# Optimization experiments

Measured on AMD Instinct MI355X. Metric: run time of the kernel, lower is better.

The kernel has to match this reference:

```python
import jax, jax.numpy as jnp
import numpy as np

N_NODES = 100000
N_EDGES = 1600000
DIM = 64

def setup_inputs() -> dict:
    key = jax.random.key(0)
    k1, k2, k3 = jax.random.split(key, 3)
    x = jax.random.normal(k1, (N_NODES, DIM), dtype=jnp.float32)
    edge_index = jax.random.randint(k2, (2, N_EDGES), 0, N_NODES, dtype=jnp.int64)
    edge_weight = jax.random.uniform(k3, (N_EDGES,), dtype=jnp.float32)
    return {"x": x, "edge_index": edge_index, "edge_weight": edge_weight}

def reference(x, edge_index, edge_weight):
    # out[row] += x[col] * edge_weight  (edge-weighted gather + scatter-add)
    row, col = edge_index[0], edge_index[1]
    messages = x[col] * edge_weight[:, None]            # [E, dim]
    out = jax.ops.segment_sum(messages, row, num_segments=x.shape[0])  # [N, dim]
    return out
```

## Files before the change

### kernel.cpp

```cpp
#include <hip/hip_runtime.h>
#include <hip/hip_fp16.h>
#include <stdint.h>


typedef unsigned long long ull;
typedef int   v4i __attribute__((ext_vector_type(4)));
typedef float v4f __attribute__((ext_vector_type(4)));

#define RB      64
#define CAP     1280
#define CHUNK   2048
#define SLOTS   48
#define BPAD    16
#define OVF_CAP 65536
#define MAXNB   2048

__device__ __forceinline__ unsigned short f2bf(float f) {
    union { float f; unsigned int u; } c;
    c.f = f;
    unsigned int lsb = (c.u >> 16) & 1u;
    c.u += 0x7fffu + lsb;
    return (unsigned short)(c.u >> 16);
}
__device__ __forceinline__ float bf2f(unsigned short u) {
    union { unsigned int u; float f; } c;
    c.u = ((unsigned int)u) << 16;
    return c.f;
}
__device__ __forceinline__ unsigned pack_cw(int col, float w) {
    unsigned hb = __half_as_ushort(__float2half(w));
    return (((unsigned)col) << 15) | (hb >> 1);
}
__device__ __forceinline__ float unpack_w(unsigned v) {
    return __half2float(__ushort_as_half((unsigned short)((v & 0x7fffu) << 1)));
}

__global__ __launch_bounds__(512) void prep(
    const int* __restrict__ ei, const float* __restrict__ ew,
    int* __restrict__ bcnt, ull* __restrict__ seg,
    int* __restrict__ ovf_cnt, int3* __restrict__ ovf, int E, int NB,
    int nbin, const float* __restrict__ x, unsigned short* __restrict__ xb,
    int n4)
{
    __shared__ int hist[MAXNB];
    __shared__ int gbase[MAXNB];
    int t = threadIdx.x;

    if ((int)blockIdx.x >= nbin) {
        int i0 = ((int)blockIdx.x - nbin) * 2048 + t;
#pragma unroll
        for (int k = 0; k < 4; ++k) {
            int i = i0 + k * 512;
            if (i < n4) {
                v4f v = ((const v4f*)x)[i];
                ushort4 o;
                o.x = f2bf(v.x); o.y = f2bf(v.y);
                o.z = f2bf(v.z); o.w = f2bf(v.w);
                ((ushort4*)xb)[i] = o;
            }
        }
        return;
    }

    for (int i = t; i < NB; i += 512) hist[i] = 0;
    __syncthreads();

    int e0 = blockIdx.x * CHUNK;
    int eb = e0 + t * 4;
    bool al4 = ((E & 3) == 0);

    unsigned pk[4];
    ull      cw[4];
    bool     vd[4];
    {
        v4i r4, c4; v4f w4;
        if (al4 && eb + 3 < E) {
            r4 = *(const v4i*)(ei + eb);
            c4 = *(const v4i*)(ei + E + eb);
            w4 = *(const v4f*)(ew + eb);
        } else {
#pragma unroll
            for (int u = 0; u < 4; ++u) {
                int e = eb + u;
                r4[u] = e < E ? ei[e] : 0;
                c4[u] = e < E ? ei[E + e] : 0;
                w4[u] = e < E ? ew[e] : 0.f;
            }
        }
#pragma unroll
        for (int u = 0; u < 4; ++u) {
            int e = eb + u;
            vd[u] = e < E;
            int bkt = r4[u] >> 6;
            int rl  = r4[u] & (RB - 1);
            int lp = 0;
            if (vd[u]) lp = atomicAdd(&hist[bkt], 1);
            pk[u] = (((unsigned)lp) << 11) | (unsigned)bkt;
            cw[u] = (((ull)__float_as_uint(w4[u])) << 32) |
                    (unsigned)((rl << 17) | c4[u]);
        }
    }
    __syncthreads();

    for (int i = t; i < NB; i += 512) {
        int h = hist[i];
        gbase[i] = h ? atomicAdd(&bcnt[i * BPAD], h) : 0;
    }
    __syncthreads();

#pragma unroll
    for (int j = 0; j < 4; ++j) {
        if (!vd[j]) continue;
        int bkt = pk[j] & 2047;
        int pos = gbase[bkt] + (int)(pk[j] >> 11);
        if (pos < CAP) {
            seg[(size_t)bkt * CAP + pos] = cw[j];
        } else {
            int o = atomicAdd(ovf_cnt, 1);
            if (o < OVF_CAP) {
                unsigned lo = (unsigned)cw[j];
                ovf[o] = make_int3((bkt << 6) | ((lo >> 17) & (RB - 1)),
                                   lo & 0x1FFFF, (int)(cw[j] >> 32));
            }
        }
    }
}

template <bool BF>
__global__ __launch_bounds__(256, 8) void bucket_acc(
    const void* __restrict__ xv, const ull* __restrict__ seg,
    const int* __restrict__ bcnt, float* __restrict__ out,
    int* __restrict__ ovf_cnt, int3* __restrict__ ovf, int N)
{
    __shared__ int      cur[RB];
    __shared__ unsigned tile[RB * SLOTS];
    int t = threadIdx.x;
    int g = blockIdx.x;
    if (t < RB) cur[t] = 0;
    __syncthreads();

    int c = bcnt[g * BPAD];
    if (c > CAP) c = CAP;
    const ull* base = seg + (size_t)g * CAP;

    for (int i = t; i < c; i += 256) {
        ull e = base[i];
        unsigned lo = (unsigned)e;
        int rl  = (lo >> 17) & (RB - 1);
        int col = lo & 0x1FFFF;
        float w = __int_as_float((int)(e >> 32));
        int pos = atomicAdd(&cur[rl], 1);
        if (pos < SLOTS) {
            tile[rl * SLOTS + pos] = pack_cw(col, w);
        } else {
            int o = atomicAdd(ovf_cnt, 1);
            if (o < OVF_CAP)
                ovf[o] = make_int3(g * RB + rl, col, __float_as_int(w));
        }
    }
    __syncthreads();

    int wid  = t >> 6;
    int lane = t & 63;
    const unsigned short* xh = (const unsigned short*)xv;
    const float*          xf = (const float*)xv;

    for (int k = 0; k < 16; ++k) {
        int r   = wid * 16 + k;
        int row = g * RB + r;
        if (row >= N) break;
        int cc = cur[r];
        if (cc > SLOTS) cc = SLOTS;
        const unsigned* tb = &tile[r * SLOTS];

        float acc = 0.0f;
        int p = 0;
        for (; p + 8 <= cc; p += 8) {
            unsigned a[8]; float xr[8];
#pragma unroll
            for (int i = 0; i < 8; ++i) a[i] = tb[p + i];
#pragma unroll
            for (int i = 0; i < 8; ++i) {
                size_t off = (((size_t)(a[i] >> 15)) << 6) + lane;
                xr[i] = BF ? bf2f(xh[off]) : xf[off];
            }
#pragma unroll
            for (int i = 0; i < 8; ++i)
                acc = fmaf(xr[i], unpack_w(a[i]), acc);
        }
        if (p < cc) {
            unsigned a[8]; float xr[8], w[8];
#pragma unroll
            for (int i = 0; i < 8; ++i) {
                int q = p + i;
                bool valid = q < cc;
                if (!valid) q = cc - 1;
                a[i] = tb[q];
                w[i] = valid ? unpack_w(a[i]) : 0.0f;
            }
#pragma unroll
            for (int i = 0; i < 8; ++i) {
                size_t off = (((size_t)(a[i] >> 15)) << 6) + lane;
                xr[i] = BF ? bf2f(xh[off]) : xf[off];
            }
#pragma unroll
            for (int i = 0; i < 8; ++i) acc = fmaf(xr[i], w[i], acc);
        }
        __builtin_nontemporal_store(acc, out + (((size_t)row) << 6) + lane);
    }
}

template <bool BF>
__global__ __launch_bounds__(256) void ovf_apply(
    const void* __restrict__ xv, const int* __restrict__ ovf_cnt,
    const int3* __restrict__ ovf, float* __restrict__ out)
{
    int n = *ovf_cnt;
    if (n > OVF_CAP) n = OVF_CAP;
    int wid  = (blockIdx.x * 256 + threadIdx.x) >> 6;
    int lane = threadIdx.x & 63;
    int nw   = gridDim.x * 4;
    for (int o = wid; o < n; o += nw) {
        int3 tt = ovf[o];
        float w = __int_as_float(tt.z);
        size_t off = (((size_t)tt.y) << 6) + lane;
        float x = BF ? bf2f(((const unsigned short*)xv)[off])
                     : ((const float*)xv)[off];
        atomicAdd(&out[(((size_t)tt.x) << 6) + lane], x * w);
    }
}

__global__ __launch_bounds__(256) void scatter_edges(
    const float* __restrict__ x, const int* __restrict__ ei,
    const float* __restrict__ ew, float* __restrict__ out, int E)
{
    long long idx = (long long)blockIdx.x * 256 + threadIdx.x;
    int e = (int)(idx >> 4);
    if (e >= E) return;
    int j = (int)(idx & 15);
    int row = ei[e];
    int col = ei[E + e];
    float w = ew[e];
    v4f v = *(const v4f*)(x + (((size_t)col) << 6) + (j << 2));
    float* op = out + (((size_t)row) << 6) + (j << 2);
    atomicAdd(op + 0, v.x * w);
    atomicAdd(op + 1, v.y * w);
    atomicAdd(op + 2, v.z * w);
    atomicAdd(op + 3, v.w * w);
}

extern "C" void kernel_launch(void* const* d_in, const int* in_sizes, int n_in,
                              void* d_out, int out_size, void* d_ws, size_t ws_size,
                              hipStream_t stream) {
    const float* x  = (const float*)d_in[0];
    const int*   ei = (const int*)d_in[1];
    const float* ew = (const float*)d_in[2];
    float*       out = (float*)d_out;

    int E = in_sizes[2];
    int N = out_size / 64;
    int NB = (N + RB - 1) / RB;

    size_t ovf_base  = (size_t)NB * BPAD + 2;
    size_t xb_base   = (ovf_base + 3 * (size_t)OVF_CAP + 3) & ~(size_t)3;
    size_t xb_ints   = (size_t)N * 32;
    size_t seg_ints  = (size_t)NB * CAP * 2;

    size_t seg_base_bf = (xb_base + xb_ints + 1) & ~(size_t)1;
    size_t need_bf     = (seg_base_bf + seg_ints) * 4;

    size_t seg_base_f  = (xb_base + 1) & ~(size_t)1;
    size_t need_f      = (seg_base_f + seg_ints) * 4;

    int nbin  = (E + CHUNK - 1) / CHUNK;
    int n4    = (N * 64) / 4;
    int nconv = (n4 + 2047) / 2048;

    if ((ws_size >= need_bf || ws_size >= need_f) && N <= (1 << 17)) {
        bool use_bf = ws_size >= need_bf;
        int* w32 = (int*)d_ws;
        int* bcnt = w32;
        int* ovf_cnt = w32 + NB * BPAD;
        int3* ovf = (int3*)(w32 + ovf_base);
        unsigned short* xb = (unsigned short*)(w32 + xb_base);
        ull* seg = (ull*)(w32 + (use_bf ? seg_base_bf : seg_base_f));

        (void)hipMemsetAsync(w32, 0, ((size_t)NB * BPAD + 2) * sizeof(int),
                             stream);

        if (use_bf) {
            prep<<<nbin + nconv, 512, 0, stream>>>(
                ei, ew, bcnt, seg, ovf_cnt, ovf, E, NB, nbin, x, xb, n4);
            bucket_acc<true><<<NB, 256, 0, stream>>>(
                xb, seg, bcnt, out, ovf_cnt, ovf, N);
            ovf_apply<true><<<64, 256, 0, stream>>>(xb, ovf_cnt, ovf, out);
        } else {
            prep<<<nbin, 512, 0, stream>>>(
                ei, ew, bcnt, seg, ovf_cnt, ovf, E, NB, nbin, x, xb, 0);
            bucket_acc<false><<<NB, 256, 0, stream>>>(
                x, seg, bcnt, out, ovf_cnt, ovf, N);
            ovf_apply<false><<<64, 256, 0, stream>>>(x, ovf_cnt, ovf, out);
        }
    } else {
        (void)hipMemsetAsync(out, 0, (size_t)out_size * sizeof(float), stream);
        long long threads = (long long)E * 16;
        scatter_edges<<<(int)((threads + 255) / 256), 256, 0, stream>>>(
            x, ei, ew, out, E);
    }
}
```

Measured before the change: 196.1 us.

## Locally sort edges by bucket in shared memory before coalesced segment writes

The binning kernel now does a block-local counting sort. It runs a prefix scan over the bucket histogram, stages edges in shared memory ordered by bucket, then writes them to the global segment array in contiguous runs instead of as scattered 8-byte stores. Bucket size doubles to 128 rows and each block handles 4096 edges at 8 per thread, and the accumulate kernel moves to 512 threads. This raises shared-memory use and block size in both kernels, which may reduce occupancy. The hidden accumulate body must also handle RB=128 correctly with a 48-slot tile per row.

```diff
diff --git a/kernel.cpp b/kernel.cpp
--- a/kernel.cpp
+++ b/kernel.cpp
@@ -7,13 +7,14 @@
 typedef int   v4i __attribute__((ext_vector_type(4)));
 typedef float v4f __attribute__((ext_vector_type(4)));
 
-#define RB      64
-#define CAP     1280
-#define CHUNK   2048
+#define RB      128
+#define CAP     2432
+#define CHUNK   4096
+#define EPT     8
 #define SLOTS   48
 #define BPAD    16
 #define OVF_CAP 65536
-#define MAXNB   2048
+#define NBP     1024
 
 __device__ __forceinline__ unsigned short f2bf(float f) {
     union { float f; unsigned int u; } c;
@@ -42,14 +43,18 @@
     int nbin, const float* __restrict__ x, unsigned short* __restrict__ xb,
     int n4)
 {
-    __shared__ int hist[MAXNB];
-    __shared__ int gbase[MAXNB];
+    __shared__ int      hist[NBP];
+    __shared__ int      lstart[NBP];
+    __shared__ int      gbase[NBP];
+    __shared__ int      wsum[8];
+    __shared__ ull      sorted[CHUNK];
+    __shared__ unsigned gpos[CHUNK];
     int t = threadIdx.x;
 
     if ((int)blockIdx.x >= nbin) {
-        int i0 = ((int)blockIdx.x - nbin) * 2048 + t;
-#pragma unroll
-        for (int k = 0; k < 4; ++k) {
+        int i0 = ((int)blockIdx.x - nbin) * 4096 + t;
+#pragma unroll
+        for (int k = 0; k < 8; ++k) {
             int i = i0 + k * 512;
             if (i < n4) {
                 v4f v = ((const v4f*)x)[i];
@@ -62,17 +67,20 @@
         return;
     }
 
-    for (int i = t; i < NB; i += 512) hist[i] = 0;
-    __syncthreads();
-
-    int e0 = blockIdx.x * CHUNK;
-    int eb = e0 + t * 4;
+    for (int i = t; i < NBP; i += 512) hist[i] = 0;
+    __syncthreads();
+
+    int e0   = blockIdx.x * CHUNK;
+    int nval = E - e0; if (nval > CHUNK) nval = CHUNK;
     bool al4 = ((E & 3) == 0);
 
-    unsigned pk[4];
-    ull      cw[4];
-    bool     vd[4];
-    {
+    int      rk[EPT];
+    unsigned bk[EPT];
+    ull      cw[EPT];
+    bool     vd[EPT];
+#pragma unroll
+    for (int j = 0; j < EPT / 4; ++j) {
+        int eb = e0 + (j * 512 + t) * 4;
         v4i r4, c4; v4f w4;
         if (al4 && eb + 3 < E) {
             r4 = *(const v4i*)(ei + eb);
@@ -89,18 +97,46 @@
         }
 #pragma unroll
         for (int u = 0; u < 4; ++u) {
+            int idx = j * 4 + u;
             int e = eb + u;
-            vd[u] = e < E;
-            int bkt = r4[u] >> 6;
+            vd[idx] = e < E;
+            int bkt = r4[u] >> 7;
             int rl  = r4[u] & (RB - 1);
-            int lp = 0;
-            if (vd[u]) lp = atomicAdd(&hist[bkt], 1);
-            pk[u] = (((unsigned)lp) << 11) | (unsigned)bkt;
-            cw[u] = (((ull)__float_as_uint(w4[u])) << 32) |
-                    (unsigned)((rl << 17) | c4[u]);
-        }
-    }
-    __syncthreads();
+            rk[idx] = vd[idx] ? atomicAdd(&hist[bkt], 1) : 0;
+            bk[idx] = (unsigned)bkt;
+            cw[idx] = (((ull)__float_as_uint(w4[u])) << 32) |
+                      (unsigned)((rl << 17) | c4[u]);
+        }
+    }
+    __syncthreads();
+
+    {
+        int a = hist[2 * t], b = hist[2 * t + 1];
+        int ps = a + b;
+        int lane = t & 63, wid = t >> 6;
+        int s = ps;
+#pragma unroll
+        for (int off = 1; off < 64; off <<= 1) {
+            int o = __shfl_up(s, off);
+            if (lane >= off) s += o;
+        }
+        if (lane == 63) wsum[wid] = s;
+        __syncthreads();
+        if (t < 8) {
+            int v = wsum[t];
+            int s2 = v;
+#pragma unroll
+            for (int off = 1; off < 8; off <<= 1) {
+                int o = __shfl_up(s2, off);
+                if (t >= off) s2 += o;
+            }
+            wsum[t] = s2 - v;
+        }
+        __syncthreads();
+        int excl = s - ps + wsum[wid];
+        lstart[2 * t]     = excl;
+        lstart[2 * t + 1] = excl + a;
+    }
 
     for (int i = t; i < NB; i += 512) {
         int h = hist[i];
@@ -109,25 +145,34 @@
     __syncthreads();
 
 #pragma unroll
-    for (int j = 0; j < 4; ++j) {
+    for (int j = 0; j < EPT; ++j) {
         if (!vd[j]) continue;
-        int bkt = pk[j] & 2047;
-        int pos = gbase[bkt] + (int)(pk[j] >> 11);
-        if (pos < CAP) {
-            seg[(size_t)bkt * CAP + pos] = cw[j];
+        int bkt = (int)bk[j];
+        int lp  = lstart[bkt] + rk[j];
+        sorted[lp] = cw[j];
+        int loc = gbase[bkt] + rk[j];
+        if (loc < CAP) {
+            gpos[lp] = (unsigned)(bkt * CAP + loc);
         } else {
+            gpos[lp] = 0xFFFFFFFFu;
             int o = atomicAdd(ovf_cnt, 1);
             if (o < OVF_CAP) {
                 unsigned lo = (unsigned)cw[j];
-                ovf[o] = make_int3((bkt << 6) | ((lo >> 17) & (RB - 1)),
+                ovf[o] = make_int3(bkt * RB + ((lo >> 17) & (RB - 1)),
                                    lo & 0x1FFFF, (int)(cw[j] >> 32));
             }
         }
     }
+    __syncthreads();
+
+    for (int i = t; i < nval; i += 512) {
+        unsigned gp = gpos[i];
+        if (gp != 0xFFFFFFFFu) seg[gp] = sorted[i];
+    }
 }
 
 template <bool BF>
-__global__ __launch_bounds__(256, 8) void bucket_acc(
+__global__ __launch_bounds__(512, 8) void bucket_acc(
     const void* __restrict__ xv, const ull* __restrict__ seg,
     const int* __restrict__ bcnt, float* __restrict__ out,
     int* __restrict__ ovf_cnt, int3* __restrict__ ovf, int N)
@@ -143,7 +188,7 @@
     if (c > CAP) c = CAP;
     const ull* base = seg + (size_t)g * CAP;
 
-    for (int i = t; i < c; i += 256) {
+    for (int i = t; i < c; i += 512) {
         ull e = base[i];
         unsigned lo = (unsigned)e;
         int rl  = (lo >> 17) & (RB - 1);
@@ -274,7 +319,7 @@
 
     int nbin  = (E + CHUNK - 1) / CHUNK;
     int n4    = (N * 64) / 4;
-    int nconv = (n4 + 2047) / 2048;
+    int nconv = (n4 + 4095) / 4096;
 
     if ((ws_size >= need_bf || ws_size >= need_f) && N <= (1 << 17)) {
         bool use_bf = ws_size >= need_bf;
@@ -291,13 +336,13 @@
         if (use_bf) {
             prep<<<nbin + nconv, 512, 0, stream>>>(
                 ei, ew, bcnt, seg, ovf_cnt, ovf, E, NB, nbin, x, xb, n4);
-            bucket_acc<true><<<NB, 256, 0, stream>>>(
+            bucket_acc<true><<<NB, 512, 0, stream>>>(
                 xb, seg, bcnt, out, ovf_cnt, ovf, N);
             ovf_apply<true><<<64, 256, 0, stream>>>(xb, ovf_cnt, ovf, out);
         } else {
             prep<<<nbin, 512, 0, stream>>>(
                 ei, ew, bcnt, seg, ovf_cnt, ovf, E, NB, nbin, x, xb, 0);
-            bucket_acc<false><<<NB, 256, 0, stream>>>(
+            bucket_acc<false><<<NB, 512, 0, stream>>>(
                 x, seg, bcnt, out, ovf_cnt, ovf, N);
             ovf_apply<false><<<64, 256, 0, stream>>>(x, ovf_cnt, ovf, out);
         }
```

After: 168.3 us. 1.17x faster.
